# Kernel tuning notes

Hardware: AMD Instinct MI355X
Metric: run time of the kernel (lower is better)

Reference implementation:

```python
import jax, jax.numpy as jnp
import numpy as np

N = 50000      # nodes
E = 800000     # edges
F_IN = 128     # num_features
H = 64         # hidden_dim
NE = 3         # num_experts
G = 64         # graphs in batch
NC = 3         # num_classes
EPS = 1e-5


def setup_inputs() -> dict:
    key = jax.random.key(0)
    ks = jax.random.split(key, 10)
    def w(k, shape, fan):
        return (jax.random.normal(k, shape, jnp.float32) / np.sqrt(fan)).astype(jnp.float32)
    return dict(
        x=jax.random.normal(ks[0], (N, F_IN), jnp.float32),
        edge_index=jax.random.randint(ks[1], (2, E), 0, N),
        batch=jnp.sort(jax.random.randint(ks[2], (N,), 0, G)),
        W_exp=w(ks[3], (NE, F_IN, H), F_IN), b_exp=jnp.zeros((NE, H), jnp.float32),
        gate_W1=w(ks[4], (F_IN, H // 2), F_IN), gate_b1=jnp.zeros((H // 2,), jnp.float32),
        gate_W2=w(ks[5], (H // 2, NE), H // 2), gate_b2=jnp.zeros((NE,), jnp.float32),
        W2=w(ks[6], (H, H), H), b2=jnp.zeros((H,), jnp.float32),
        bn1_g=jnp.ones((H,), jnp.float32), bn1_b=jnp.zeros((H,), jnp.float32),
        bn2_g=jnp.ones((H,), jnp.float32), bn2_b=jnp.zeros((H,), jnp.float32),
        cls_W=w(ks[7], (3 * H, NC), 3 * H), cls_b=jnp.zeros((NC,), jnp.float32),
    )


def _gcn_prop(h, src, dst, deg_isqrt, deg_inv):
    # GCN propagation with self-loops: out_i = sum_{j->i} d_j^-1/2 d_i^-1/2 h_j + d_i^-1 h_i
    bshape = (-1,) + (1,) * (h.ndim - 1)
    norm = (deg_isqrt[src] * deg_isqrt[dst]).reshape(bshape)
    agg = jax.ops.segment_sum(h[src] * norm, dst, num_segments=N)
    return agg + h * deg_inv.reshape(bshape)


def _bn(h, g, b):
    # training-mode batch norm over the node dimension (biased variance)
    mu = h.mean(0)
    var = h.var(0)
    return (h - mu) * jax.lax.rsqrt(var + EPS) * g + b


def reference(x, edge_index, batch, W_exp, b_exp, gate_W1, gate_b1, gate_W2, gate_b2,
              W2, b2, bn1_g, bn1_b, bn2_g, bn2_b, cls_W, cls_b):
    src, dst = edge_index[0], edge_index[1]
    deg = jax.ops.segment_sum(jnp.ones((E,), jnp.float32), dst, num_segments=N) + 1.0
    deg_isqrt = jax.lax.rsqrt(deg)
    deg_inv = 1.0 / deg

    # gating network: softmax over experts, per node
    gate = jax.nn.softmax(jnp.maximum(x @ gate_W1 + gate_b1, 0.0) @ gate_W2 + gate_b2, axis=1)  # [N, NE]

    # all experts vectorized: transform then propagate [N, NE, H]
    h = jnp.einsum('nf,efh->neh', x, W_exp)
    h = _gcn_prop(h, src, dst, deg_isqrt, deg_inv) + b_exp
    h = jnp.einsum('ne,neh->nh', gate, h)  # gated combine

    h = jnp.maximum(_bn(h, bn1_g, bn1_b), 0.0)
    # dropout is identity in eval mode
    h = _gcn_prop(h @ W2, src, dst, deg_isqrt, deg_inv) + b2
    h = jnp.maximum(_bn(h, bn2_g, bn2_b), 0.0)

    cnt = jax.ops.segment_sum(jnp.ones((N,), jnp.float32), batch, num_segments=G)
    x_sum = jax.ops.segment_sum(h, batch, num_segments=G)
    x_mean = x_sum / jnp.maximum(cnt, 1.0)[:, None]
    x_max = jax.ops.segment_max(h, batch, num_segments=G)
    z = jnp.concatenate([x_mean, x_max, x_sum], axis=1)  # [G, 3H]
    return z @ cls_W + cls_b
```

## Files before the change

kernel.cpp:

```cpp
#include <hip/hip_runtime.h>

#define N_NODES 50000
#define N_EDGES 800000
#define F 128
#define HDIM 64
#define NE 3
#define NGRAPH 64
#define NC 3
#define BN_EPS 1e-5f
#define NBLK_A 200
#define NBUCK 196
#define NBLK_EXP 782
#define NBLK_GY 1563

typedef __attribute__((ext_vector_type(8))) short short8;
typedef __attribute__((ext_vector_type(4))) float f32x4;

__device__ inline unsigned short f2bf(float f) {
    unsigned int u = __float_as_uint(f);
    unsigned int r = (u + 0x7FFFu + ((u >> 16) & 1u)) >> 16;
    return (unsigned short)r;
}
__device__ inline float bf2f(unsigned short u) {
    return __uint_as_float(((unsigned int)u) << 16);
}

__global__ __launch_bounds__(256) void k_prep(const float* __restrict__ Wexp,
        const float* __restrict__ gW1, const int* __restrict__ batch,
        const int* __restrict__ dst,
        unsigned short* __restrict__ wpack, unsigned short* __restrict__ gwpack,
        int* __restrict__ gstart, int* __restrict__ bh, float* __restrict__ zbase) {
    int b = blockIdx.x, tid = threadIdx.x;
    if (b < 12) {
        int t0 = b * 256 + tid;
        int f = t0 >> 6, l = t0 & 63;
        int e = f >> 4, t = (f >> 2) & 3, kk = f & 3;
        int h = t * 16 + (l & 15);
        int kbase = kk * 32 + (l >> 4) * 8;
        short8 o;
        #pragma unroll
        for (int j = 0; j < 8; ++j)
            o[j] = (short)f2bf(Wexp[e * (F * HDIM) + (kbase + j) * HDIM + h]);
        ((short8*)wpack)[f * 64 + l] = o;
    } else if (b == 12) {
        for (int t0 = tid; t0 < 8 * 64; t0 += 256) {
            int f = t0 >> 6, l = t0 & 63;
            int t = f >> 2, kk = f & 3;
            int h = t * 16 + (l & 15);
            int kbase = kk * 32 + (l >> 4) * 8;
            short8 o;
            #pragma unroll
            for (int j = 0; j < 8; ++j)
                o[j] = (short)f2bf(gW1[(kbase + j) * 32 + h]);
            ((short8*)gwpack)[f * 64 + l] = o;
        }
    } else if (b == 13) {
        int g = tid;
        if (g <= NGRAPH) {
            int lo = 0, hi = N_NODES;
            while (lo < hi) { int m = (lo + hi) >> 1; if (batch[m] < g) lo = m + 1; else hi = m; }
            gstart[g] = lo;
        }
    } else if (b < 14 + NBLK_A) {
        __shared__ int hist[256];
        hist[tid] = 0;
        __syncthreads();
        int base = (b - 14) * 4000;
        for (int i = tid; i < 4000; i += 256)
            atomicAdd(&hist[dst[base + i] >> 8], 1);
        __syncthreads();
        bh[(b - 14) * 256 + tid] = hist[tid];
    } else {
        int idx = (b - 14 - NBLK_A) * 256 + tid;
        if (idx < 8192) zbase[idx] = 0.f;
    }
}

__global__ __launch_bounds__(256) void k_bscan(int* __restrict__ bh, int* __restrict__ bucketbase,
                                               int* __restrict__ row_start) {
    int b = threadIdx.x;
    int sum = 0;
    #pragma unroll 4
    for (int k = 0; k < NBLK_A; ++k) {
        int v = bh[k * 256 + b];
        bh[k * 256 + b] = sum;
        sum += v;
    }
    int lane = b & 63, wid = b >> 6;
    __shared__ int wsums[4];
    int xsc = sum;
    #pragma unroll
    for (int off = 1; off < 64; off <<= 1) {
        int u = __shfl_up(xsc, off, 64);
        if (lane >= off) xsc += u;
    }
    if (lane == 63) wsums[wid] = xsc;
    __syncthreads();
    int woff = 0;
    for (int wq = 0; wq < wid; ++wq) woff += wsums[wq];
    int excl = woff + xsc - sum;
    bucketbase[b] = excl;
    if (b == 255) {
        bucketbase[256] = excl + sum;
        row_start[N_NODES] = excl + sum;
    }
}

__global__ __launch_bounds__(256) void k_bplace(const int* __restrict__ ei, const int* __restrict__ bh,
        const int* __restrict__ bucketbase, int2* __restrict__ pairs) {
    __shared__ int cur[256];
    int tid = threadIdx.x;
    cur[tid] = bucketbase[tid] + bh[blockIdx.x * 256 + tid];
    __syncthreads();
    int base = blockIdx.x * 4000;
    for (int i = tid; i < 4000; i += 256) {
        int e = base + i;
        int s = ei[e], d = ei[N_EDGES + e];
        int slot = atomicAdd(&cur[d >> 8], 1);
        pairs[slot] = make_int2(s, d);
    }
}

__global__ __launch_bounds__(256) void k_bfinal(const int2* __restrict__ pairs,
        const int* __restrict__ bucketbase, int* __restrict__ row_start,
        float* __restrict__ deg_isqrt, int* __restrict__ csr_src) {
    __shared__ int deg[256];
    __shared__ int cur[256];
    __shared__ int wsums[4];
    int b = blockIdx.x, t = threadIdx.x;
    int beg = bucketbase[b], end = bucketbase[b + 1];
    deg[t] = 0;
    __syncthreads();
    for (int i = beg + t; i < end; i += 256)
        atomicAdd(&deg[pairs[i].y & 255], 1);
    __syncthreads();
    int d = deg[t];
    int lane = t & 63, wid = t >> 6;
    int xsc = d;
    #pragma unroll
    for (int off = 1; off < 64; off <<= 1) {
        int u = __shfl_up(xsc, off, 64);
        if (lane >= off) xsc += u;
    }
    if (lane == 63) wsums[wid] = xsc;
    __syncthreads();
    int woff = 0;
    for (int wq = 0; wq < wid; ++wq) woff += wsums[wq];
    int rs = beg + woff + xsc - d;
    int node = b * 256 + t;
    if (node < N_NODES) {
        row_start[node] = rs;
        deg_isqrt[node] = rsqrtf((float)d + 1.0f);
    }
    cur[t] = rs;
    __syncthreads();
    for (int i = beg + t; i < end; i += 256) {
        int2 p = pairs[i];
        int slot = atomicAdd(&cur[p.y & 255], 1);
        csr_src[slot] = p.x;
    }
}

__global__ __launch_bounds__(256) void k_gateM(const float* __restrict__ x,
        const float* __restrict__ deg_isqrt, const unsigned short* __restrict__ gwpack,
        const float* __restrict__ gb1, const float* __restrict__ gW2,
        const float* __restrict__ gb2, float* __restrict__ gate,
        unsigned short* __restrict__ xpb1) {
    int tid = threadIdx.x;
    int w = tid >> 6, l = tid & 63;
    int lo = l & 15, hi = l >> 4;
    int n0 = blockIdx.x * 64 + w * 16;
    int nlo = n0 + lo;
    bool vrow = nlo < N_NODES;
    int arow = vrow ? nlo : N_NODES - 1;
    float si = deg_isqrt[arow];
    short8 a[4];
    #pragma unroll
    for (int kk = 0; kk < 4; ++kk) {
        int c4 = (kk * 32 + hi * 8) >> 2;
        float4 v0 = ((const float4*)x)[(size_t)arow * 32 + c4];
        float4 v1 = ((const float4*)x)[(size_t)arow * 32 + c4 + 1];
        short8 t8;
        t8[0] = (short)f2bf(v0.x); t8[1] = (short)f2bf(v0.y);
        t8[2] = (short)f2bf(v0.z); t8[3] = (short)f2bf(v0.w);
        t8[4] = (short)f2bf(v1.x); t8[5] = (short)f2bf(v1.y);
        t8[6] = (short)f2bf(v1.z); t8[7] = (short)f2bf(v1.w);
        a[kk] = t8;
        if (vrow) {
            ushort4 o0, o1;
            o0.x = f2bf(v0.x * si); o0.y = f2bf(v0.y * si);
            o0.z = f2bf(v0.z * si); o0.w = f2bf(v0.w * si);
            o1.x = f2bf(v1.x * si); o1.y = f2bf(v1.y * si);
            o1.z = f2bf(v1.z * si); o1.w = f2bf(v1.w * si);
            ((ushort4*)xpb1)[(size_t)arow * 32 + c4]     = o0;
            ((ushort4*)xpb1)[(size_t)arow * 32 + c4 + 1] = o1;
        }
    }
    const short8* gw8 = (const short8*)gwpack;
    f32x4 acc0 = {0.f, 0.f, 0.f, 0.f}, acc1 = {0.f, 0.f, 0.f, 0.f};
    #pragma unroll
    for (int kk = 0; kk < 4; ++kk) {
        acc0 = __builtin_amdgcn_mfma_f32_16x16x32_bf16(a[kk], gw8[kk * 64 + l], acc0, 0, 0, 0);
        acc1 = __builtin_amdgcn_mfma_f32_16x16x32_bf16(a[kk], gw8[(4 + kk) * 64 + l], acc1, 0, 0, 0);
    }
    float b1a = gb1[lo], b1b = gb1[16 + lo];
    float w20[3], w21[3];
    #pragma unroll
    for (int e = 0; e < 3; ++e) { w20[e] = gW2[lo * 3 + e]; w21[e] = gW2[(16 + lo) * 3 + e]; }
    float bb0 = gb2[0], bb1 = gb2[1], bb2 = gb2[2];
    #pragma unroll
    for (int r = 0; r < 4; ++r) {
        float h0 = fmaxf(acc0[r] + b1a, 0.f);
        float h1 = fmaxf(acc1[r] + b1b, 0.f);
        float le[3];
        #pragma unroll
        for (int e = 0; e < 3; ++e) {
            float p = fmaf(h0, w20[e], h1 * w21[e]);
            p += __shfl_xor(p, 1, 64);
            p += __shfl_xor(p, 2, 64);
            p += __shfl_xor(p, 4, 64);
            p += __shfl_xor(p, 8, 64);
            le[e] = p;
        }
        le[0] += bb0; le[1] += bb1; le[2] += bb2;
        float m = fmaxf(le[0], fmaxf(le[1], le[2]));
        float e0 = __expf(le[0] - m), e1 = __expf(le[1] - m), e2 = __expf(le[2] - m);
        float inv = 1.f / (e0 + e1 + e2);
        int n = n0 + hi * 4 + r;
        if (n < N_NODES && lo < 3) {
            float gg = (lo == 0) ? e0 * inv : (lo == 1 ? e1 * inv : e2 * inv);
            gate[n * 3 + lo] = gg;
        }
    }
}

__global__ __launch_bounds__(256) void k_gsum_x(const int* __restrict__ csr_src,
        const int* __restrict__ row_start, const float* __restrict__ deg_isqrt,
        const unsigned short* __restrict__ hin, unsigned short* __restrict__ out) {
    int lane = threadIdx.x & 15;
    int grp  = threadIdx.x >> 4;
    int n = blockIdx.x * 16 + grp;
    if (n >= N_NODES) return;
    const short8* h8 = (const short8*)hin;
    int beg = row_start[n], end = row_start[n + 1];
    short8 sv = h8[(size_t)n * 16 + lane];
    float a[8];
    #pragma unroll
    for (int j = 0; j < 8; ++j) a[j] = bf2f((unsigned short)sv[j]);
    int e = beg;
    for (; e + 3 < end; e += 4) {
        int s0 = csr_src[e], s1 = csr_src[e + 1], s2 = csr_src[e + 2], s3 = csr_src[e + 3];
        short8 v0 = h8[(size_t)s0 * 16 + lane];
        short8 v1 = h8[(size_t)s1 * 16 + lane];
        short8 v2 = h8[(size_t)s2 * 16 + lane];
        short8 v3 = h8[(size_t)s3 * 16 + lane];
        #pragma unroll
        for (int j = 0; j < 8; ++j)
            a[j] += (bf2f((unsigned short)v0[j]) + bf2f((unsigned short)v1[j]))
                  + (bf2f((unsigned short)v2[j]) + bf2f((unsigned short)v3[j]));
    }
    for (; e < end; ++e) {
        short8 v0 = h8[(size_t)csr_src[e] * 16 + lane];
        #pragma unroll
        for (int j = 0; j < 8; ++j) a[j] += bf2f((unsigned short)v0[j]);
    }
    float s = deg_isqrt[n];
    short8 o;
    #pragma unroll
    for (int j = 0; j < 8; ++j) o[j] = (short)f2bf(a[j] * s);
    ((short8*)out)[(size_t)n * 16 + lane] = o;
}

__global__ __launch_bounds__(256) void k_expert(const unsigned short* __restrict__ xp,
        const unsigned short* __restrict__ wpack, const float* __restrict__ bexp,
        const float* __restrict__ gate, unsigned short* __restrict__ h1preb,
        float* __restrict__ partial1) {
    int tid = threadIdx.x;
    int w = tid >> 6, l = tid & 63;
    int n0 = blockIdx.x * 64 + w * 16;
    int lo = l & 15, hi = l >> 4;
    int arow = n0 + lo; if (arow >= N_NODES) arow = N_NODES - 1;
    const short8* xr = (const short8*)xp + (size_t)arow * 16;
    short8 a0 = xr[hi], a1 = xr[4 + hi], a2 = xr[8 + hi], a3 = xr[12 + hi];
    const short8* wp8 = (const short8*)wpack;
    float comb[4][4];
    #pragma unroll
    for (int t = 0; t < 4; ++t)
        #pragma unroll
        for (int r = 0; r < 4; ++r) comb[t][r] = 0.f;
    int nrow[4];
    #pragma unroll
    for (int r = 0; r < 4; ++r) {
        int n = n0 + hi * 4 + r;
        nrow[r] = (n < N_NODES) ? n : -1;
    }
    #pragma unroll
    for (int e = 0; e < NE; ++e) {
        float g_[4];
        #pragma unroll
        for (int r = 0; r < 4; ++r) g_[r] = (nrow[r] >= 0) ? gate[nrow[r] * 3 + e] : 0.f;
        #pragma unroll
        for (int t = 0; t < 4; ++t) {
            int fbase = (e * 16 + t * 4) * 64 + l;
            f32x4 acc = {0.f, 0.f, 0.f, 0.f};
            acc = __builtin_amdgcn_mfma_f32_16x16x32_bf16(a0, wp8[fbase      ], acc, 0, 0, 0);
            acc = __builtin_amdgcn_mfma_f32_16x16x32_bf16(a1, wp8[fbase +  64], acc, 0, 0, 0);
            acc = __builtin_amdgcn_mfma_f32_16x16x32_bf16(a2, wp8[fbase + 128], acc, 0, 0, 0);
            acc = __builtin_amdgcn_mfma_f32_16x16x32_bf16(a3, wp8[fbase + 192], acc, 0, 0, 0);
            float be = bexp[e * HDIM + t * 16 + lo];
            #pragma unroll
            for (int r = 0; r < 4; ++r) comb[t][r] = fmaf(g_[r], acc[r] + be, comb[t][r]);
        }
    }
    __shared__ float sred[4][128];
    #pragma unroll
    for (int t = 0; t < 4; ++t) {
        float s = 0.f, q = 0.f;
        #pragma unroll
        for (int r = 0; r < 4; ++r) {
            if (nrow[r] >= 0) {
                float v = comb[t][r];
                h1preb[(size_t)nrow[r] * HDIM + t * 16 + lo] = f2bf(v);
                s += v; q = fmaf(v, v, q);
            }
        }
        s += __shfl_xor(s, 16, 64); s += __shfl_xor(s, 32, 64);
        q += __shfl_xor(q, 16, 64); q += __shfl_xor(q, 32, 64);
        if (hi == 0) {
            sred[w][t * 16 + lo] = s;
            sred[w][64 + t * 16 + lo] = q;
        }
    }
    __syncthreads();
    if (tid < 128)
        partial1[blockIdx.x * 128 + tid] =
            sred[0][tid] + sred[1][tid] + sred[2][tid] + sred[3][tid];
}

__global__ __launch_bounds__(256) void k_colred(const float* __restrict__ partial, int nblk,
                                                float* __restrict__ sums) {
    int c = blockIdx.x;
    int tid = threadIdx.x;
    float s = 0.f;
    for (int k = tid; k < nblk; k += 256)
        s += partial[(size_t)k * 128 + c];
    __shared__ float red[256];
    red[tid] = s;
    __syncthreads();
    #pragma unroll
    for (int off = 128; off >= 1; off >>= 1) {
        if (tid < off) red[tid] += red[tid + off];
        __syncthreads();
    }
    if (tid == 0) sums[c] = red[0];
}

__global__ __launch_bounds__(256) void k_w2(const unsigned short* __restrict__ h1preb,
        const float* __restrict__ sums, const float* __restrict__ bng, const float* __restrict__ bnb,
        const float* __restrict__ W2, const float* __restrict__ deg_isqrt,
        unsigned short* __restrict__ y) {
    __shared__ float scsh_s[128];
    __shared__ float4 hsd[64 * 16];
    __shared__ float  wsd[64 * 64];
    int tid = threadIdx.x;
    if (tid < 64) {
        float mu = sums[tid] * (1.0f / N_NODES);
        float var = sums[64 + tid] * (1.0f / N_NODES) - mu * mu;
        float rs = rsqrtf(var + BN_EPS);
        float sc = rs * bng[tid];
        scsh_s[tid] = sc;
        scsh_s[64 + tid] = bnb[tid] - mu * sc;
    }
    int nbase = blockIdx.x * 64;
    for (int i = tid; i < 64 * 16; i += 256) ((float4*)wsd)[i] = ((const float4*)W2)[i];
    __syncthreads();
    for (int i = tid; i < 64 * 8; i += 256) {
        int r = i >> 3, c8 = i & 7;
        int n = nbase + r; if (n >= N_NODES) n = N_NODES - 1;
        short8 v8 = ((const short8*)h1preb)[(size_t)n * 8 + c8];
        float vv[8];
        #pragma unroll
        for (int j = 0; j < 8; ++j) {
            int col = c8 * 8 + j;
            vv[j] = fmaxf(fmaf(bf2f((unsigned short)v8[j]), scsh_s[col], scsh_s[64 + col]), 0.f);
        }
        hsd[r * 16 + c8 * 2]     = make_float4(vv[0], vv[1], vv[2], vv[3]);
        hsd[r * 16 + c8 * 2 + 1] = make_float4(vv[4], vv[5], vv[6], vv[7]);
    }
    __syncthreads();
    int h = tid & 63, iq = tid >> 6;
    float acc[16];
    #pragma unroll
    for (int i = 0; i < 16; ++i) acc[i] = 0.f;
    for (int k4 = 0; k4 < 16; ++k4) {
        float w0 = wsd[(k4 * 4 + 0) * 64 + h];
        float w1 = wsd[(k4 * 4 + 1) * 64 + h];
        float w2v = wsd[(k4 * 4 + 2) * 64 + h];
        float w3 = wsd[(k4 * 4 + 3) * 64 + h];
        #pragma unroll
        for (int i = 0; i < 16; ++i) {
            float4 xv = hsd[(iq * 16 + i) * 16 + k4];
            acc[i] = fmaf(xv.x, w0, acc[i]);
            acc[i] = fmaf(xv.y, w1, acc[i]);
            acc[i] = fmaf(xv.z, w2v, acc[i]);
            acc[i] = fmaf(xv.w, w3, acc[i]);
        }
    }
    #pragma unroll
    for (int i = 0; i < 16; ++i) {
        int n = nbase + iq * 16 + i;
        if (n < N_NODES) y[(size_t)n * 64 + h] = f2bf(acc[i] * deg_isqrt[n]);
    }
}

__global__ __launch_bounds__(256) void k_gsum_y(const int* __restrict__ csr_src,
        const int* __restrict__ row_start, const float* __restrict__ deg_isqrt,
        const unsigned short* __restrict__ hin, float* __restrict__ out,
        float* __restrict__ partial2) {
    int tid = threadIdx.x;
    int lane8 = tid & 7;
    int grp = tid >> 3;
    int n = blockIdx.x * 32 + grp;
    bool valid = n < N_NODES;
    int nn = valid ? n : N_NODES - 1;
    const short8* h8 = (const short8*)hin;
    int beg = row_start[nn], end = row_start[nn + 1];
    short8 sv = h8[(size_t)nn * 8 + lane8];
    float a[8];
    #pragma unroll
    for (int j = 0; j < 8; ++j) a[j] = bf2f((unsigned short)sv[j]);
    int e = beg;
    for (; e + 3 < end; e += 4) {
        int s0 = csr_src[e], s1 = csr_src[e + 1], s2 = csr_src[e + 2], s3 = csr_src[e + 3];
        short8 v0 = h8[(size_t)s0 * 8 + lane8];
        short8 v1 = h8[(size_t)s1 * 8 + lane8];
        short8 v2 = h8[(size_t)s2 * 8 + lane8];
        short8 v3 = h8[(size_t)s3 * 8 + lane8];
        #pragma unroll
        for (int j = 0; j < 8; ++j)
            a[j] += (bf2f((unsigned short)v0[j]) + bf2f((unsigned short)v1[j]))
                  + (bf2f((unsigned short)v2[j]) + bf2f((unsigned short)v3[j]));
    }
    for (; e < end; ++e) {
        short8 v0 = h8[(size_t)csr_src[e] * 8 + lane8];
        #pragma unroll
        for (int j = 0; j < 8; ++j) a[j] += bf2f((unsigned short)v0[j]);
    }
    float s = deg_isqrt[nn];
    float o[8];
    #pragma unroll
    for (int j = 0; j < 8; ++j) o[j] = a[j] * s;
    if (valid) {
        ((float4*)out)[(size_t)n * 16 + lane8 * 2]     = make_float4(o[0], o[1], o[2], o[3]);
        ((float4*)out)[(size_t)n * 16 + lane8 * 2 + 1] = make_float4(o[4], o[5], o[6], o[7]);
    }
    float ss[8], sq[8];
    #pragma unroll
    for (int j = 0; j < 8; ++j) {
        float v = valid ? o[j] : 0.f;
        ss[j] = v; sq[j] = v * v;
    }
    #pragma unroll
    for (int j = 0; j < 8; ++j) {
        ss[j] += __shfl_xor(ss[j], 8, 64);  sq[j] += __shfl_xor(sq[j], 8, 64);
        ss[j] += __shfl_xor(ss[j], 16, 64); sq[j] += __shfl_xor(sq[j], 16, 64);
        ss[j] += __shfl_xor(ss[j], 32, 64); sq[j] += __shfl_xor(sq[j], 32, 64);
    }
    __shared__ float sred[4][128];
    int wv = tid >> 6;
    if (((tid >> 3) & 7) == 0) {
        #pragma unroll
        for (int j = 0; j < 8; ++j) {
            sred[wv][lane8 * 8 + j] = ss[j];
            sred[wv][64 + lane8 * 8 + j] = sq[j];
        }
    }
    __syncthreads();
    if (tid < 128)
        partial2[blockIdx.x * 128 + tid] =
            sred[0][tid] + sred[1][tid] + sred[2][tid] + sred[3][tid];
}

__global__ __launch_bounds__(256) void k_pool(const float* __restrict__ xp2,
        const float* __restrict__ sums, const float* __restrict__ bng, const float* __restrict__ bnb,
        const int* __restrict__ gstart,
        float* __restrict__ psum, unsigned int* __restrict__ pmax) {
    __shared__ float scsh_s[128];
    int tid = threadIdx.x;
    if (tid < 64) {
        float mu = sums[tid] * (1.0f / N_NODES);
        float var = sums[64 + tid] * (1.0f / N_NODES) - mu * mu;
        float rs = rsqrtf(var + BN_EPS);
        float sc = rs * bng[tid];
        scsh_s[tid] = sc;
        scsh_s[64 + tid] = bnb[tid] - mu * sc;
    }
    __syncthreads();
    int g = blockIdx.x >> 2, ck = blockIdx.x & 3;
    int h = tid & 63, q = tid >> 6;
    int s0 = gstart[g], s1 = gstart[g + 1];
    int len = s1 - s0;
    int cbeg = s0 + (len * ck) / 4;
    int cend = s0 + (len * (ck + 1)) / 4;
    float sc = scsh_s[h], sh = scsh_s[64 + h];
    float ls = 0.f, lm = 0.f;
    for (int r = cbeg + q; r < cend; r += 4) {
        float v = fmaxf(fmaf(xp2[(size_t)r * 64 + h], sc, sh), 0.f);
        ls += v; lm = fmaxf(lm, v);
    }
    __shared__ float red[2][4][64];
    red[0][q][h] = ls; red[1][q][h] = lm;
    __syncthreads();
    if (q == 0) {
        ls = red[0][0][h] + red[0][1][h] + red[0][2][h] + red[0][3][h];
        lm = fmaxf(fmaxf(red[1][0][h], red[1][1][h]), fmaxf(red[1][2][h], red[1][3][h]));
        atomicAdd(&psum[g * 64 + h], ls);
        atomicMax(&pmax[g * 64 + h], __float_as_uint(lm));
    }
}

__global__ void k_cls(const float* __restrict__ psum, const unsigned int* __restrict__ pmax,
                      const int* __restrict__ gstart, const float* __restrict__ Wc,
                      const float* __restrict__ bc, float* __restrict__ out) {
    int t = threadIdx.x;
    if (t >= NGRAPH * NC) return;
    int g = t / NC, c = t % NC;
    float cnt = (float)(gstart[g + 1] - gstart[g]);
    float invc = 1.f / fmaxf(cnt, 1.f);
    float acc = bc[c];
    #pragma unroll 8
    for (int j = 0; j < 64; ++j) {
        float s = psum[g * 64 + j];
        float mx = __uint_as_float(pmax[g * 64 + j]);
        acc = fmaf(s * invc, Wc[j * 3 + c], acc);
        acc = fmaf(mx, Wc[(64 + j) * 3 + c], acc);
        acc = fmaf(s, Wc[(128 + j) * 3 + c], acc);
    }
    out[g * NC + c] = acc;
}

extern "C" void kernel_launch(void* const* d_in, const int* in_sizes, int n_in,
                              void* d_out, int out_size, void* d_ws, size_t ws_size,
                              hipStream_t stream) {
    const float* x    = (const float*)d_in[0];
    const int*   ei   = (const int*)d_in[1];
    const int*   batch= (const int*)d_in[2];
    const float* Wexp = (const float*)d_in[3];
    const float* bexp = (const float*)d_in[4];
    const float* gW1  = (const float*)d_in[5];
    const float* gb1  = (const float*)d_in[6];
    const float* gW2  = (const float*)d_in[7];
    const float* gb2  = (const float*)d_in[8];
    const float* W2   = (const float*)d_in[9];
    const float* bn1g = (const float*)d_in[11];
    const float* bn1b = (const float*)d_in[12];
    const float* bn2g = (const float*)d_in[13];
    const float* bn2b = (const float*)d_in[14];
    const float* clsW = (const float*)d_in[15];
    const float* clsb = (const float*)d_in[16];
    float* out = (float*)d_out;

    float* ws = (float*)d_ws;
    const size_t NN = N_NODES;
    float* deg_isqrt = ws;
    float* gate      = ws + NN;
    unsigned short* xpb1   = (unsigned short*)(ws + 4 * NN);
    unsigned short* xpb    = (unsigned short*)(ws + 68 * NN);
    unsigned short* h1preb = (unsigned short*)(ws + 132 * NN);
    unsigned short* ypb    = (unsigned short*)(ws + 164 * NN);
    float* xp2       = ws + 196 * NN;
    float* stats     = ws + 260 * NN;
    float* sums1 = stats + 256;
    float* sums2 = stats + 384;
    float* psum  = stats + 512;
    unsigned int* pmax = (unsigned int*)(stats + 512 + 4096);
    int* gstart  = (int*)(stats + 512 + 8192);
    float* partial1 = stats + 16384;
    float* partial2 = partial1 + 131072;
    int* row_start  = (int*)(partial2 + 262144);
    int* bh         = row_start + NN + 8;
    int* bucketbase = bh + NBLK_A * 256;
    int* csr_src    = bucketbase + 264;
    int2* pairs     = (int2*)(csr_src + N_EDGES);
    unsigned short* wpack  = (unsigned short*)(pairs + N_EDGES);
    unsigned short* gwpack = wpack + 24576;

    k_prep<<<14 + NBLK_A + 32, 256, 0, stream>>>(Wexp, gW1, batch, ei + N_EDGES,
                                                 wpack, gwpack, gstart, bh, psum);
    k_bscan<<<1, 256, 0, stream>>>(bh, bucketbase, row_start);
    k_bplace<<<NBLK_A, 256, 0, stream>>>(ei, bh, bucketbase, pairs);
    k_bfinal<<<NBUCK, 256, 0, stream>>>(pairs, bucketbase, row_start, deg_isqrt, csr_src);

    k_gateM<<<NBLK_EXP, 256, 0, stream>>>(x, deg_isqrt, gwpack, gb1, gW2, gb2, gate, xpb1);
    k_gsum_x<<<(N_NODES + 15) / 16, 256, 0, stream>>>(csr_src, row_start, deg_isqrt, xpb1, xpb);
    k_expert<<<NBLK_EXP, 256, 0, stream>>>(xpb, wpack, bexp, gate, h1preb, partial1);
    k_colred<<<128, 256, 0, stream>>>(partial1, NBLK_EXP, sums1);
    k_w2<<<NBLK_EXP, 256, 0, stream>>>(h1preb, sums1, bn1g, bn1b, W2, deg_isqrt, ypb);
    k_gsum_y<<<NBLK_GY, 256, 0, stream>>>(csr_src, row_start, deg_isqrt, ypb, xp2, partial2);
    k_colred<<<128, 256, 0, stream>>>(partial2, NBLK_GY, sums2);
    k_pool<<<NGRAPH * 4, 256, 0, stream>>>(xp2, sums2, bn2g, bn2b, gstart, psum, pmax);
    k_cls<<<1, 256, 0, stream>>>(psum, pmax, gstart, clsW, clsb, out);
}
```

Baseline: 168.4 us.

## Store second-layer output as bf16 and fuse classifier into pooling kernel

The second propagation now writes its pre-BN output in bf16 instead of fp32, halving that intermediate's write and read traffic. The pooling kernel uses one block per graph and computes the classifier output directly, which removes the k_cls launch, the global atomics and the zero-init blocks in k_prep. In exchange, each pooling block now processes a whole graph with 64 blocks instead of 256, which lowers parallelism in that stage, and bf16 rounding adds precision loss before BN2 and pooling.

Result: slower. 204.6 us (+21.5%).

```diff
diff --git a/kernel.cpp b/kernel.cpp
--- a/kernel.cpp
+++ b/kernel.cpp
@@ -29,7 +29,7 @@
         const float* __restrict__ gW1, const int* __restrict__ batch,
         const int* __restrict__ dst,
         unsigned short* __restrict__ wpack, unsigned short* __restrict__ gwpack,
-        int* __restrict__ gstart, int* __restrict__ bh, float* __restrict__ zbase) {
+        int* __restrict__ gstart, int* __restrict__ bh) {
     int b = blockIdx.x, tid = threadIdx.x;
     if (b < 12) {
         int t0 = b * 256 + tid;
@@ -61,7 +61,7 @@
             while (lo < hi) { int m = (lo + hi) >> 1; if (batch[m] < g) lo = m + 1; else hi = m; }
             gstart[g] = lo;
         }
-    } else if (b < 14 + NBLK_A) {
+    } else {
         __shared__ int hist[256];
         hist[tid] = 0;
         __syncthreads();
@@ -70,9 +70,6 @@
             atomicAdd(&hist[dst[base + i] >> 8], 1);
         __syncthreads();
         bh[(b - 14) * 256 + tid] = hist[tid];
-    } else {
-        int idx = (b - 14 - NBLK_A) * 256 + tid;
-        if (idx < 8192) zbase[idx] = 0.f;
     }
 }
 
@@ -415,7 +412,7 @@
 
 __global__ __launch_bounds__(256) void k_gsum_y(const int* __restrict__ csr_src,
         const int* __restrict__ row_start, const float* __restrict__ deg_isqrt,
-        const unsigned short* __restrict__ hin, float* __restrict__ out,
+        const unsigned short* __restrict__ hin, unsigned short* __restrict__ out,
         float* __restrict__ partial2) {
     int tid = threadIdx.x;
     int lane8 = tid & 7;
@@ -451,8 +448,10 @@
     #pragma unroll
     for (int j = 0; j < 8; ++j) o[j] = a[j] * s;
     if (valid) {
-        ((float4*)out)[(size_t)n * 16 + lane8 * 2]     = make_float4(o[0], o[1], o[2], o[3]);
-        ((float4*)out)[(size_t)n * 16 + lane8 * 2 + 1] = make_float4(o[4], o[5], o[6], o[7]);
+        short8 ob;
+        #pragma unroll
+        for (int j = 0; j < 8; ++j) ob[j] = (short)f2bf(o[j]);
+        ((short8*)out)[(size_t)n * 8 + lane8] = ob;
     }
     float ss[8], sq[8];
     #pragma unroll
@@ -481,11 +480,13 @@
             sred[0][tid] + sred[1][tid] + sred[2][tid] + sred[3][tid];
 }
 
-__global__ __launch_bounds__(256) void k_pool(const float* __restrict__ xp2,
+__global__ __launch_bounds__(256) void k_pool(const unsigned short* __restrict__ xp2b,
         const float* __restrict__ sums, const float* __restrict__ bng, const float* __restrict__ bnb,
-        const int* __restrict__ gstart,
-        float* __restrict__ psum, unsigned int* __restrict__ pmax) {
+        const int* __restrict__ gstart, const float* __restrict__ Wc,
+        const float* __restrict__ bc, float* __restrict__ out) {
     __shared__ float scsh_s[128];
+    __shared__ float red[2][4][64];
+    __shared__ float ps[64], pm[64];
     int tid = threadIdx.x;
     if (tid < 64) {
         float mu = sums[tid] * (1.0f / N_NODES);
@@ -496,47 +497,38 @@
         scsh_s[64 + tid] = bnb[tid] - mu * sc;
     }
     __syncthreads();
-    int g = blockIdx.x >> 2, ck = blockIdx.x & 3;
+    int g = blockIdx.x;
     int h = tid & 63, q = tid >> 6;
     int s0 = gstart[g], s1 = gstart[g + 1];
-    int len = s1 - s0;
-    int cbeg = s0 + (len * ck) / 4;
-    int cend = s0 + (len * (ck + 1)) / 4;
     float sc = scsh_s[h], sh = scsh_s[64 + h];
     float ls = 0.f, lm = 0.f;
-    for (int r = cbeg + q; r < cend; r += 4) {
-        float v = fmaxf(fmaf(xp2[(size_t)r * 64 + h], sc, sh), 0.f);
+    for (int r = s0 + q; r < s1; r += 4) {
+        float v = fmaxf(fmaf(bf2f(xp2b[(size_t)r * 64 + h]), sc, sh), 0.f);
         ls += v; lm = fmaxf(lm, v);
     }
-    __shared__ float red[2][4][64];
     red[0][q][h] = ls; red[1][q][h] = lm;
     __syncthreads();
-    if (q == 0) {
-        ls = red[0][0][h] + red[0][1][h] + red[0][2][h] + red[0][3][h];
-        lm = fmaxf(fmaxf(red[1][0][h], red[1][1][h]), fmaxf(red[1][2][h], red[1][3][h]));
-        atomicAdd(&psum[g * 64 + h], ls);
-        atomicMax(&pmax[g * 64 + h], __float_as_uint(lm));
-    }
-}
-
-__global__ void k_cls(const float* __restrict__ psum, const unsigned int* __restrict__ pmax,
-                      const int* __restrict__ gstart, const float* __restrict__ Wc,
-                      const float* __restrict__ bc, float* __restrict__ out) {
-    int t = threadIdx.x;
-    if (t >= NGRAPH * NC) return;
-    int g = t / NC, c = t % NC;
-    float cnt = (float)(gstart[g + 1] - gstart[g]);
-    float invc = 1.f / fmaxf(cnt, 1.f);
-    float acc = bc[c];
-    #pragma unroll 8
-    for (int j = 0; j < 64; ++j) {
-        float s = psum[g * 64 + j];
-        float mx = __uint_as_float(pmax[g * 64 + j]);
-        acc = fmaf(s * invc, Wc[j * 3 + c], acc);
-        acc = fmaf(mx, Wc[(64 + j) * 3 + c], acc);
-        acc = fmaf(s, Wc[(128 + j) * 3 + c], acc);
-    }
-    out[g * NC + c] = acc;
+    if (tid < 64) {
+        ps[tid] = red[0][0][tid] + red[0][1][tid] + red[0][2][tid] + red[0][3][tid];
+        pm[tid] = fmaxf(fmaxf(red[1][0][tid], red[1][1][tid]),
+                        fmaxf(red[1][2][tid], red[1][3][tid]));
+    }
+    __syncthreads();
+    int c = tid >> 6, j = tid & 63;
+    if (c < NC) {
+        float cnt = (float)(s1 - s0);
+        float invc = 1.f / fmaxf(cnt, 1.f);
+        float contrib = ps[j] * invc * Wc[j * 3 + c]
+                      + pm[j] * Wc[(64 + j) * 3 + c]
+                      + ps[j] * Wc[(128 + j) * 3 + c];
+        contrib += __shfl_xor(contrib, 1, 64);
+        contrib += __shfl_xor(contrib, 2, 64);
+        contrib += __shfl_xor(contrib, 4, 64);
+        contrib += __shfl_xor(contrib, 8, 64);
+        contrib += __shfl_xor(contrib, 16, 64);
+        contrib += __shfl_xor(contrib, 32, 64);
+        if (j == 0) out[g * NC + c] = contrib + bc[c];
+    }
 }
 
 extern "C" void kernel_launch(void* const* d_in, const int* in_sizes, int n_in,
@@ -568,12 +560,10 @@
     unsigned short* xpb    = (unsigned short*)(ws + 68 * NN);
     unsigned short* h1preb = (unsigned short*)(ws + 132 * NN);
     unsigned short* ypb    = (unsigned short*)(ws + 164 * NN);
-    float* xp2       = ws + 196 * NN;
+    unsigned short* xp2b   = (unsigned short*)(ws + 196 * NN);
     float* stats     = ws + 260 * NN;
     float* sums1 = stats + 256;
     float* sums2 = stats + 384;
-    float* psum  = stats + 512;
-    unsigned int* pmax = (unsigned int*)(stats + 512 + 4096);
     int* gstart  = (int*)(stats + 512 + 8192);
     float* partial1 = stats + 16384;
     float* partial2 = partial1 + 131072;
@@ -585,8 +575,8 @@
     unsigned short* wpack  = (unsigned short*)(pairs + N_EDGES);
     unsigned short* gwpack = wpack + 24576;
 
-    k_prep<<<14 + NBLK_A + 32, 256, 0, stream>>>(Wexp, gW1, batch, ei + N_EDGES,
-                                                 wpack, gwpack, gstart, bh, psum);
+    k_prep<<<14 + NBLK_A, 256, 0, stream>>>(Wexp, gW1, batch, ei + N_EDGES,
+                                            wpack, gwpack, gstart, bh);
     k_bscan<<<1, 256, 0, stream>>>(bh, bucketbase, row_start);
     k_bplace<<<NBLK_A, 256, 0, stream>>>(ei, bh, bucketbase, pairs);
     k_bfinal<<<NBUCK, 256, 0, stream>>>(pairs, bucketbase, row_start, deg_isqrt, csr_src);
@@ -596,8 +586,7 @@
     k_expert<<<NBLK_EXP, 256, 0, stream>>>(xpb, wpack, bexp, gate, h1preb, partial1);
     k_colred<<<128, 256, 0, stream>>>(partial1, NBLK_EXP, sums1);
     k_w2<<<NBLK_EXP, 256, 0, stream>>>(h1preb, sums1, bn1g, bn1b, W2, deg_isqrt, ypb);
-    k_gsum_y<<<NBLK_GY, 256, 0, stream>>>(csr_src, row_start, deg_isqrt, ypb, xp2, partial2);
+    k_gsum_y<<<NBLK_GY, 256, 0, stream>>>(csr_src, row_start, deg_isqrt, ypb, xp2b, partial2);
     k_colred<<<128, 256, 0, stream>>>(partial2, NBLK_GY, sums2);
-    k_pool<<<NGRAPH * 4, 256, 0, stream>>>(xp2, sums2, bn2g, bn2b, gstart, psum, pmax);
-    k_cls<<<1, 256, 0, stream>>>(psum, pmax, gstart, clsW, clsb, out);
-}
+    k_pool<<<NGRAPH, 256, 0, stream>>>(xp2b, sums2, bn2g, bn2b, gstart, clsW, clsb, out);
+}
```
